# Kernel tuning notes

Hardware: AMD Instinct MI355X
Metric: run time of the kernel (lower is better)

The kernel has to match this reference:

```python
import jax, jax.numpy as jnp
import numpy as np

B, S, H = 32, 2048, 1024


def setup_inputs() -> dict:
    key = jax.random.key(0)
    k1, k2, k3, k4, k5, k6 = jax.random.split(key, 6)
    hidden = jax.random.normal(k1, (B, H), dtype=jnp.float32)
    encoder_outputs = jax.random.normal(k2, (B, S, H), dtype=jnp.float32)
    lengths = jax.random.randint(k3, (B,), 1, S + 1, dtype=jnp.int64)
    scale = 1.0 / np.sqrt(H)
    Wq = jax.random.normal(k4, (H, H), dtype=jnp.float32) * scale
    Wk = jax.random.normal(k5, (H, H), dtype=jnp.float32) * scale
    v = jax.random.uniform(k6, (H,), dtype=jnp.float32)  # torch.rand init
    return {"hidden": hidden, "encoder_outputs": encoder_outputs,
            "lengths": lengths, "Wq": Wq, "Wk": Wk, "v": v}


def reference(hidden, encoder_outputs, lengths, Wq, Wk, v):
    # query: (B, 1, H); nn.Linear(bias=False) applies x @ W.T
    query = (hidden @ Wq.T)[:, None, :]
    keys = jnp.einsum('bsh,kh->bsk', encoder_outputs, Wk)  # (B, S, H)
    energy = jnp.tanh(query + keys)                         # (B, S, H)
    attn = jnp.einsum('bsh,h->bs', energy, v)               # (B, S)
    seq = encoder_outputs.shape[1]
    mask = jnp.arange(seq)[None, :] < lengths[:, None]      # (B, S)
    attn = jnp.where(mask, attn, -jnp.inf)
    return jax.nn.softmax(attn, axis=1)
```

## Files before the change

### kernel.cpp

```cpp
#include <hip/hip_runtime.h>
#include <hip/hip_fp16.h>
#include <stdint.h>

#define B_SZ 32
#define S_SZ 2048
#define H_SZ 1024
#define M_SZ (B_SZ * S_SZ)

typedef _Float16 half8 __attribute__((ext_vector_type(8)));
typedef float floatx4 __attribute__((ext_vector_type(4)));

struct h4 { _Float16 x, y, z, w; };

__global__ __launch_bounds__(256) void convert_f32_to_f16(
    const float* __restrict__ in, h4* __restrict__ out, int n4) {
  int i = blockIdx.x * blockDim.x + threadIdx.x;
  int stride = gridDim.x * blockDim.x;
  const float4* in4 = (const float4*)in;
  for (; i < n4; i += stride) {
    float4 f = in4[i];
    h4 o;
    o.x = (_Float16)f.x; o.y = (_Float16)f.y;
    o.z = (_Float16)f.z; o.w = (_Float16)f.w;
    out[i] = o;
  }
}

__global__ __launch_bounds__(256) void query_kernel(
    const float* __restrict__ hidden, const float* __restrict__ Wq,
    float* __restrict__ q) {
  int t = blockIdx.x * blockDim.x + threadIdx.x;
  int b = t & 31;
  int n = t >> 5;
  const float4* h4p = (const float4*)(hidden + (size_t)b * H_SZ);
  const float4* w4p = (const float4*)(Wq + (size_t)n * H_SZ);
  float acc = 0.f;
  #pragma unroll 4
  for (int i = 0; i < H_SZ / 4; ++i) {
    float4 h = h4p[i], w = w4p[i];
    acc = fmaf(h.x, w.x, acc);
    acc = fmaf(h.y, w.y, acc);
    acc = fmaf(h.z, w.z, acc);
    acc = fmaf(h.w, w.w, acc);
  }
  q[(size_t)b * H_SZ + n] = acc;
}

__device__ __forceinline__ void gl_lds16(const void* g, void* l) {
  __builtin_amdgcn_global_load_lds(
      (const __attribute__((address_space(1))) void*)g,
      (__attribute__((address_space(3))) void*)l,
      16, 0, 0);
}

__device__ __forceinline__ float fast_tanh(float x) {
  float ax = fabsf(x);
  float e = __expf(ax * -2.0f);
  float t = (1.0f - e) / (1.0f + e);
  return copysignf(t, x);
}

#define TILE 128
#define BK 32

__global__ __launch_bounds__(256, 4) void fused_keys_kernel(
    const float* __restrict__ A,
    const _Float16* __restrict__ Bt,
    const float* __restrict__ q,
    const float* __restrict__ v,
    float* __restrict__ partial)
{
  __shared__ __align__(16) _Float16 As[2][TILE * BK];
  __shared__ __align__(16) _Float16 Bs[2][TILE * BK];
  __shared__ float q_l[TILE];
  __shared__ float v_l[TILE];

  const int tid  = threadIdx.x;
  const int w    = tid >> 6;
  const int lane = tid & 63;

  const int hw   = blockIdx.x;
  const int xcd  = hw & 7;
  const int slot = hw >> 3;
  const int bn   = slot & 7;
  const int bm   = ((slot >> 3) << 3) | xcd;

  const int R0   = bm * TILE;
  const int C0   = bn * TILE;
  const int bidx = R0 >> 11;

  if (tid < TILE) {
    q_l[tid] = q[(size_t)bidx * H_SZ + C0 + tid];
    v_l[tid] = v[C0 + tid];
  }

  const int cL   = lane & 15, quad = lane >> 4;
  const int sB   = (cL >> 1) & 3;

  floatx4 acc[2][8];
  #pragma unroll
  for (int m = 0; m < 2; ++m)
    #pragma unroll
    for (int n = 0; n < 8; ++n)
      acc[m][n] = (floatx4){0.f, 0.f, 0.f, 0.f};

  const int arow = w * 32 + (lane >> 1);
  const int ah   = lane & 1;
  const int akey = (lane >> 2) & 3;
  const int ap0  = (2 * ah)     ^ akey;
  const int ap1  = (2 * ah + 1) ^ akey;
  const float* Asrc = A + (size_t)(R0 + arow) * H_SZ + ah * 16;

  const int brow_l = lane >> 2;
  const int bp     = lane & 3;
  const _Float16* Bblk = Bt + (size_t)C0 * H_SZ;

  auto stageB = [&](int kt2, int b) {
    const int kof = kt2 * BK;
    #pragma unroll
    for (int j = 0; j < 2; ++j) {
      const int row = w * 32 + j * 16 + brow_l;
      const int cg  = bp ^ ((row >> 1) & 3);
      gl_lds16(Bblk + (size_t)row * H_SZ + kof + cg * 8,
               (char*)&Bs[b][0] + (w * 128 + j * 64) * 16);
    }
  };

  float4 ar[4];
  auto loadA = [&](int kt2) {
    const float4* p = (const float4*)(Asrc + kt2 * BK);
    ar[0] = p[0]; ar[1] = p[1]; ar[2] = p[2]; ar[3] = p[3];
  };

  auto writeA = [&](int b) {
    half8 h0 = (half8){(_Float16)ar[0].x, (_Float16)ar[0].y, (_Float16)ar[0].z, (_Float16)ar[0].w,
                       (_Float16)ar[1].x, (_Float16)ar[1].y, (_Float16)ar[1].z, (_Float16)ar[1].w};
    half8 h1 = (half8){(_Float16)ar[2].x, (_Float16)ar[2].y, (_Float16)ar[2].z, (_Float16)ar[2].w,
                       (_Float16)ar[3].x, (_Float16)ar[3].y, (_Float16)ar[3].z, (_Float16)ar[3].w};
    _Float16* dst = &As[b][arow * BK];
    *(half8*)(dst + ap0 * 8) = h0;
    *(half8*)(dst + ap1 * 8) = h1;
  };

  auto compute = [&](int b) {
    half8 af[2], bf[8];
    #pragma unroll
    for (int m = 0; m < 2; ++m) {
      const int r = w * 32 + m * 16 + cL;
      af[m] = *(const half8*)(&As[b][r * BK] + ((quad ^ sB) << 3));
    }
    #pragma unroll
    for (int n = 0; n < 8; ++n) {
      const int r = n * 16 + cL;
      bf[n] = *(const half8*)(&Bs[b][r * BK] + ((quad ^ sB) << 3));
    }
    #pragma unroll
    for (int m = 0; m < 2; ++m)
      #pragma unroll
      for (int n = 0; n < 8; ++n)
        acc[m][n] = __builtin_amdgcn_mfma_f32_16x16x32_f16(af[m], bf[n], acc[m][n], 0, 0, 0);
  };

  loadA(0);
  stageB(0, 0);
  writeA(0);
  __syncthreads();

  int cur = 0;
  for (int kt = 0; kt < H_SZ / BK - 1; ++kt) {
    loadA(kt + 1);
    stageB(kt + 1, cur ^ 1);
    compute(cur);
    writeA(cur ^ 1);
    __syncthreads();
    cur ^= 1;
  }
  compute(cur);

  float qv[8], vv[8];
  #pragma unroll
  for (int n = 0; n < 8; ++n) {
    const int col = n * 16 + cL;
    qv[n] = q_l[col];
    vv[n] = v_l[col];
  }
  #pragma unroll
  for (int m = 0; m < 2; ++m) {
    #pragma unroll
    for (int r = 0; r < 4; ++r) {
      float s = 0.f;
      #pragma unroll
      for (int n = 0; n < 8; ++n)
        s += vv[n] * fast_tanh(qv[n] + acc[m][n][r]);
      s += __shfl_xor(s, 1);
      s += __shfl_xor(s, 2);
      s += __shfl_xor(s, 4);
      s += __shfl_xor(s, 8);
      if (cL == 0)
        partial[(size_t)bn * M_SZ + R0 + w * 32 + m * 16 + quad * 4 + r] = s;
    }
  }
}

__global__ __launch_bounds__(256) void softmax_kernel(
    const float* __restrict__ partial, const int* __restrict__ lengths,
    float* __restrict__ out) {
  __shared__ float wred[4];
  __shared__ float wsum[4];
  const int b = blockIdx.x;
  const int tid = threadIdx.x;
  const int len = lengths[b];

  float lg[8];
  #pragma unroll
  for (int i = 0; i < 8; ++i) {
    const int s = tid + i * 256;
    const size_t row = (size_t)b * S_SZ + s;
    float l = 0.f;
    #pragma unroll
    for (int nt = 0; nt < 8; ++nt) l += partial[(size_t)nt * M_SZ + row];
    lg[i] = (s < len) ? l : -INFINITY;
  }

  float mx = lg[0];
  #pragma unroll
  for (int i = 1; i < 8; ++i) mx = fmaxf(mx, lg[i]);
  #pragma unroll
  for (int off = 32; off; off >>= 1) mx = fmaxf(mx, __shfl_xor(mx, off));
  if ((tid & 63) == 0) wred[tid >> 6] = mx;
  __syncthreads();
  mx = fmaxf(fmaxf(wred[0], wred[1]), fmaxf(wred[2], wred[3]));

  float pe[8];
  float sum = 0.f;
  #pragma unroll
  for (int i = 0; i < 8; ++i) {
    float e = (lg[i] == -INFINITY) ? 0.f : __expf(lg[i] - mx);
    pe[i] = e;
    sum += e;
  }
  #pragma unroll
  for (int off = 32; off; off >>= 1) sum += __shfl_xor(sum, off);
  if ((tid & 63) == 0) wsum[tid >> 6] = sum;
  __syncthreads();
  sum = wsum[0] + wsum[1] + wsum[2] + wsum[3];
  const float inv = 1.0f / sum;

  #pragma unroll
  for (int i = 0; i < 8; ++i) {
    const int s = tid + i * 256;
    out[(size_t)b * S_SZ + s] = pe[i] * inv;
  }
}

extern "C" void kernel_launch(void* const* d_in, const int* in_sizes, int n_in,
                              void* d_out, int out_size, void* d_ws, size_t ws_size,
                              hipStream_t stream) {
  const float* hidden  = (const float*)d_in[0];
  const float* enc     = (const float*)d_in[1];
  const int*   lengths = (const int*)d_in[2];
  const float* Wq      = (const float*)d_in[3];
  const float* Wk      = (const float*)d_in[4];
  const float* v       = (const float*)d_in[5];
  float* out = (float*)d_out;

  char* ws = (char*)d_ws;
  _Float16* B16     = (_Float16*)ws;
  float*    q       = (float*)(ws + 2097152);
  float*    partial = (float*)(ws + 2097152 + 131072);

  convert_f32_to_f16<<<1024, 256, 0, stream>>>(Wk, (h4*)B16, (H_SZ * H_SZ) / 4);
  query_kernel<<<128, 256, 0, stream>>>(hidden, Wq, q);
  fused_keys_kernel<<<(M_SZ / TILE) * (H_SZ / TILE), 256, 0, stream>>>(enc, B16, q, v, partial);
  softmax_kernel<<<B_SZ, 256, 0, stream>>>(partial, lengths, out);
}
```

Before: 610.0 us.

## Deepen GEMM pipeline with triple-buffered B, double-buffered A registers, and MFMA priority

Result: slower. 648.3 us (+6.3%).

```diff
diff --git a/kernel.cpp b/kernel.cpp
--- a/kernel.cpp
+++ b/kernel.cpp
@@ -62,8 +62,9 @@
 
 #define TILE 128
 #define BK 32
-
-__global__ __launch_bounds__(256, 4) void fused_keys_kernel(
+#define NT (H_SZ / BK)
+
+__global__ __launch_bounds__(256, 3) void fused_keys_kernel(
     const float* __restrict__ A,
     const _Float16* __restrict__ Bt,
     const float* __restrict__ q,
@@ -71,7 +72,7 @@
     float* __restrict__ partial)
 {
   __shared__ __align__(16) _Float16 As[2][TILE * BK];
-  __shared__ __align__(16) _Float16 Bs[2][TILE * BK];
+  __shared__ __align__(16) _Float16 Bs[3][TILE * BK];
   __shared__ float q_l[TILE];
   __shared__ float v_l[TILE];
 
@@ -115,6 +116,8 @@
   const int bp     = lane & 3;
   const _Float16* Bblk = Bt + (size_t)C0 * H_SZ;
 
+  float4 ar[2][4];
+
   auto stageB = [&](int kt2, int b) {
     const int kof = kt2 * BK;
     #pragma unroll
@@ -126,56 +129,66 @@
     }
   };
 
-  float4 ar[4];
-  auto loadA = [&](int kt2) {
+  auto loadA = [&](int kt2, int s) {
     const float4* p = (const float4*)(Asrc + kt2 * BK);
-    ar[0] = p[0]; ar[1] = p[1]; ar[2] = p[2]; ar[3] = p[3];
-  };
-
-  auto writeA = [&](int b) {
-    half8 h0 = (half8){(_Float16)ar[0].x, (_Float16)ar[0].y, (_Float16)ar[0].z, (_Float16)ar[0].w,
-                       (_Float16)ar[1].x, (_Float16)ar[1].y, (_Float16)ar[1].z, (_Float16)ar[1].w};
-    half8 h1 = (half8){(_Float16)ar[2].x, (_Float16)ar[2].y, (_Float16)ar[2].z, (_Float16)ar[2].w,
-                       (_Float16)ar[3].x, (_Float16)ar[3].y, (_Float16)ar[3].z, (_Float16)ar[3].w};
+    ar[s][0] = p[0]; ar[s][1] = p[1]; ar[s][2] = p[2]; ar[s][3] = p[3];
+  };
+
+  auto writeA = [&](int s, int b) {
+    half8 h0 = (half8){(_Float16)ar[s][0].x, (_Float16)ar[s][0].y, (_Float16)ar[s][0].z, (_Float16)ar[s][0].w,
+                       (_Float16)ar[s][1].x, (_Float16)ar[s][1].y, (_Float16)ar[s][1].z, (_Float16)ar[s][1].w};
+    half8 h1 = (half8){(_Float16)ar[s][2].x, (_Float16)ar[s][2].y, (_Float16)ar[s][2].z, (_Float16)ar[s][2].w,
+                       (_Float16)ar[s][3].x, (_Float16)ar[s][3].y, (_Float16)ar[s][3].z, (_Float16)ar[s][3].w};
     _Float16* dst = &As[b][arow * BK];
     *(half8*)(dst + ap0 * 8) = h0;
     *(half8*)(dst + ap1 * 8) = h1;
   };
 
-  auto compute = [&](int b) {
+  auto compute = [&](int ab, int bb) {
     half8 af[2], bf[8];
     #pragma unroll
     for (int m = 0; m < 2; ++m) {
       const int r = w * 32 + m * 16 + cL;
-      af[m] = *(const half8*)(&As[b][r * BK] + ((quad ^ sB) << 3));
+      af[m] = *(const half8*)(&As[ab][r * BK] + ((quad ^ sB) << 3));
     }
     #pragma unroll
     for (int n = 0; n < 8; ++n) {
       const int r = n * 16 + cL;
-      bf[n] = *(const half8*)(&Bs[b][r * BK] + ((quad ^ sB) << 3));
-    }
+      bf[n] = *(const half8*)(&Bs[bb][r * BK] + ((quad ^ sB) << 3));
+    }
+    __builtin_amdgcn_s_setprio(1);
     #pragma unroll
     for (int m = 0; m < 2; ++m)
       #pragma unroll
       for (int n = 0; n < 8; ++n)
         acc[m][n] = __builtin_amdgcn_mfma_f32_16x16x32_f16(af[m], bf[n], acc[m][n], 0, 0, 0);
-  };
-
-  loadA(0);
+    __builtin_amdgcn_s_setprio(0);
+  };
+
   stageB(0, 0);
-  writeA(0);
-  __syncthreads();
-
-  int cur = 0;
-  for (int kt = 0; kt < H_SZ / BK - 1; ++kt) {
-    loadA(kt + 1);
-    stageB(kt + 1, cur ^ 1);
-    compute(cur);
-    writeA(cur ^ 1);
-    __syncthreads();
-    cur ^= 1;
-  }
-  compute(cur);
+  asm volatile("" ::: "memory");
+  loadA(0, 0);
+  stageB(1, 1);
+  asm volatile("" ::: "memory");
+  loadA(1, 1);
+  writeA(0, 0);
+  asm volatile("s_waitcnt lgkmcnt(0)" ::: "memory");
+  __builtin_amdgcn_s_barrier();
+
+  #pragma unroll
+  for (int t = 0; t < NT; ++t) {
+    if (t + 2 < NT) {
+      stageB(t + 2, (t + 2) % 3);
+      asm volatile("" ::: "memory");
+      loadA(t + 2, t & 1);
+    }
+    compute(t & 1, t % 3);
+    if (t + 1 < NT) {
+      writeA((t + 1) & 1, (t + 1) & 1);
+      asm volatile("s_waitcnt lgkmcnt(0)" ::: "memory");
+      __builtin_amdgcn_s_barrier();
+    }
+  }
 
   float qv[8], vv[8];
   #pragma unroll
```
